# Kernel tuning notes

Hardware: AMD Instinct MI355X
Metric: run time of the kernel (lower is better)

The kernel has to match this reference:

```python
import jax, jax.numpy as jnp
import numpy as np

D_MODEL = 1024
NUM_HEADS = 16
THETA = 10000.0
NEG = -1000000.0  # masked_fill value used by the torch code


def _rope(x, token_positions, theta):
    # x: [B, H, S, d_head]; token_positions: [S] int
    d_k = x.shape[-1]
    half = d_k // 2
    j = jnp.arange(half, dtype=jnp.float32)
    inv_freq = theta ** (-(2.0 * j) / d_k)                      # [half]
    ang = token_positions.astype(jnp.float32)[:, None] * inv_freq  # [S, half]
    cos = jnp.cos(ang)
    sin = jnp.sin(ang)
    xp = x.reshape(x.shape[:-1] + (half, 2))  # adjacent pairs (pc, 2)
    x0, x1 = xp[..., 0], xp[..., 1]
    o0 = x0 * cos - x1 * sin
    o1 = x0 * sin + x1 * cos
    out = jnp.stack([o0, o1], axis=-1)
    return out.reshape(x.shape)


def setup_inputs() -> dict:
    key = jax.random.key(0)
    k0, k1, k2 = jax.random.split(key, 3)
    B, S, D = 2, 2048, D_MODEL
    std = (2.0 / (D + D)) ** 0.5
    X = jax.random.normal(k0, (B, S, D), dtype=jnp.float32)
    QKV_weights = jax.random.normal(k1, (3 * D, D), dtype=jnp.float32) * std
    O_weights = jax.random.normal(k2, (D, D), dtype=jnp.float32) * std
    token_positions = jnp.arange(S, dtype=jnp.int32)
    return {"X": X, "token_positions": token_positions,
            "QKV_weights": QKV_weights, "O_weights": O_weights}


def reference(X, token_positions, QKV_weights, O_weights):
    B, S, D = X.shape
    H = NUM_HEADS
    dh = D // H
    qkv = jnp.einsum('od,bsd->bso', QKV_weights, X)  # [B, S, 3D]
    Q, K, V = jnp.split(qkv, 3, axis=-1)

    def split_heads(t):
        return t.reshape(B, S, H, dh).transpose(0, 2, 1, 3)  # [B,H,S,dh]

    Q, K, V = split_heads(Q), split_heads(K), split_heads(V)
    Q = _rope(Q, token_positions, THETA)
    K = _rope(K, token_positions, THETA)

    scores = (jnp.einsum('bhqd,bhkd->bhqk', Q, K) / jnp.sqrt(jnp.float32(dh))).astype(jnp.float32)
    causal = jnp.tril(jnp.ones((S, S), dtype=bool))
    scores = jnp.where(causal, scores, NEG)
    probs = jax.nn.softmax(scores, axis=-1)
    attn = jnp.einsum('bhqk,bhkd->bhqd', probs, V.astype(jnp.float32)).astype(Q.dtype)
    attn = attn.transpose(0, 2, 1, 3).reshape(B, S, D)
    return jnp.einsum('od,bsd->bso', O_weights, attn)
```

## Files before the change

kernel.cpp:

```cpp
#include <hip/hip_runtime.h>
#include <math.h>

#define S_LEN 2048

using bf16x8  = __attribute__((ext_vector_type(8))) short;
using shortx4 = __attribute__((ext_vector_type(4))) short;
using f32x4   = __attribute__((ext_vector_type(4))) float;
using uintx4  = __attribute__((ext_vector_type(4))) unsigned;
using uintx2  = __attribute__((ext_vector_type(2))) unsigned;

static __device__ __forceinline__ short f2bf(float f) {
  unsigned u = __float_as_uint(f);
  u += 0x7fffu + ((u >> 16) & 1u);
  return (short)(u >> 16);
}

#if __has_builtin(__builtin_amdgcn_cvt_pk_bf16_f32)
using bf16x2_t = __attribute__((ext_vector_type(2))) __bf16;
static __device__ __forceinline__ unsigned pkbf(float a, float b) {
  bf16x2_t v = __builtin_amdgcn_cvt_pk_bf16_f32(a, b);
  return __builtin_bit_cast(unsigned, v);
}
#else
static __device__ __forceinline__ unsigned pkbf(float a, float b) {
  return (unsigned)(unsigned short)f2bf(a) | ((unsigned)(unsigned short)f2bf(b) << 16);
}
#endif

#define GLD_LDS16(gptr, lptr)                                                  \
  __builtin_amdgcn_global_load_lds(                                            \
      (__attribute__((address_space(1))) void*)(gptr),                         \
      (__attribute__((address_space(3))) void*)(lptr), 16, 0, 0)

#define EXP2_SHIFT 20.0f

static __device__ __forceinline__ f32x4 exp2s4(f32x4 a) {
  return (f32x4){__builtin_amdgcn_exp2f(a[0] - EXP2_SHIFT),
                 __builtin_amdgcn_exp2f(a[1] - EXP2_SHIFT),
                 __builtin_amdgcn_exp2f(a[2] - EXP2_SHIFT),
                 __builtin_amdgcn_exp2f(a[3] - EXP2_SHIFT)};
}

static __device__ __forceinline__ int sigma64(int k) {
  return (k & 0x20) | ((k & 0x0C) << 1) | ((k & 0x10) >> 2) | (k & 3);
}

__global__ __launch_bounds__(256) void init_kernel(const float* __restrict__ X,
                                                   const float* __restrict__ W1,
                                                   const float* __restrict__ W2,
                                                   const int* __restrict__ tok,
                                                   short* __restrict__ Xb,
                                                   short* __restrict__ W1b,
                                                   short* __restrict__ W2b,
                                                   float2* __restrict__ table) {
  if (blockIdx.x < 4096) {
    size_t idx = (size_t)(blockIdx.x * 256 + threadIdx.x) * 8;
    const float* src;
    short* dst;
    size_t off;
    if (idx < 4194304) { src = X; dst = Xb; off = idx; }
    else if (idx < 4194304 + 3145728) { src = W1; dst = W1b; off = idx - 4194304; }
    else { src = W2; dst = W2b; off = idx - (4194304 + 3145728); }
    float4 a = *(const float4*)(src + off);
    float4 b = *(const float4*)(src + off + 4);
    bf16x8 o = {f2bf(a.x), f2bf(a.y), f2bf(a.z), f2bf(a.w),
                f2bf(b.x), f2bf(b.y), f2bf(b.z), f2bf(b.w)};
    *(bf16x8*)(dst + off) = o;
  } else {
    int i = (blockIdx.x - 4096) * 256 + threadIdx.x;
    int s = i >> 5, j = i & 31;
    double pos = (double)tok[s];
    double ang = pos * pow(10000.0, -(double)j / 32.0);
    table[i] = make_float2((float)cos(ang), (float)sin(ang));
  }
}

template <int BM, typename OutT, int EPI>
__global__ __launch_bounds__(256) void gemm_ll(const short* __restrict__ A,
                                               const short* __restrict__ B,
                                               OutT* __restrict__ C,
                                               const float2* __restrict__ tab,
                                               short* __restrict__ Qb,
                                               short* __restrict__ Kb,
                                               short* __restrict__ Vb,
                                               int M, int N, int K) {
  constexpr int MI = BM / 32;
  constexpr int AI = BM / 64;
  __shared__ short As[BM * 32];
  __shared__ short Bs[128 * 32];
  const int tid  = threadIdx.x;
  const int lane = tid & 63;
  const int wv   = tid >> 6;
  const int wm   = (wv >> 1) * (BM / 2);
  const int wn   = (wv & 1) * 64;
  const int m16  = lane & 15;
  const int q4   = lane >> 4;
  const int rowBase = blockIdx.y * BM;
  const int colBase = blockIdx.x * 128;
  const int lrow = lane >> 2;
  const int lchk = (lane & 3) ^ ((lane >> 3) & 3);
  const int fsw  = (q4 ^ ((m16 >> 1) & 3)) * 8;

  f32x4 acc[MI][4];
#pragma unroll
  for (int i = 0; i < MI; ++i)
#pragma unroll
    for (int j = 0; j < 4; ++j) acc[i][j] = (f32x4){0.f, 0.f, 0.f, 0.f};

  const short* Agl = A + (size_t)rowBase * K;
  const short* Bgl = B + (size_t)colBase * K;

  for (int kk = 0; kk < K; kk += 32) {
#pragma unroll
    for (int i = 0; i < AI; ++i) {
      const int r0 = (wv * AI + i) * 16;
      GLD_LDS16(Agl + (size_t)(r0 + lrow) * K + kk + lchk * 8, &As[r0 * 32]);
    }
#pragma unroll
    for (int i = 0; i < 2; ++i) {
      const int r0 = (wv * 2 + i) * 16;
      GLD_LDS16(Bgl + (size_t)(r0 + lrow) * K + kk + lchk * 8, &Bs[r0 * 32]);
    }
    __syncthreads();

    bf16x8 af[MI], bfv[4];
#pragma unroll
    for (int mi = 0; mi < MI; ++mi)
      af[mi] = *(const bf16x8*)&As[(wm + mi * 16 + m16) * 32 + fsw];
#pragma unroll
    for (int ni = 0; ni < 4; ++ni)
      bfv[ni] = *(const bf16x8*)&Bs[(wn + ni * 16 + m16) * 32 + fsw];
#pragma unroll
    for (int mi = 0; mi < MI; ++mi)
#pragma unroll
      for (int ni = 0; ni < 4; ++ni)
        acc[mi][ni] = __builtin_amdgcn_mfma_f32_16x16x32_bf16(af[mi], bfv[ni], acc[mi][ni], 0, 0, 0);
    __syncthreads();
  }

  if constexpr (EPI == 0) {
#pragma unroll
    for (int mi = 0; mi < MI; ++mi)
#pragma unroll
      for (int ni = 0; ni < 4; ++ni) {
        const int rbase = rowBase + wm + mi * 16 + q4 * 4;
        const int cidx  = colBase + wn + ni * 16 + m16;
#pragma unroll
        for (int r = 0; r < 4; ++r) {
          float v = acc[mi][ni][r];
          if constexpr (sizeof(OutT) == 2)
            C[(size_t)(rbase + r) * N + cidx] = (OutT)f2bf(v);
          else
            C[(size_t)(rbase + r) * N + cidx] = (OutT)v;
        }
      }
  } else {
    const int sect = colBase >> 10;
#pragma unroll
    for (int mi = 0; mi < MI; ++mi)
#pragma unroll
      for (int ni = 0; ni < 4; ++ni) {
        const int col = colBase + wn + ni * 16 + m16;
        const int rb  = rowBase + wm + mi * 16 + q4 * 4;
        if (sect == 2) {
          const int hd = col - 2048;
#pragma unroll
          for (int r = 0; r < 4; ++r)
            Vb[(size_t)(rb + r) * 1024 + hd] = f2bf(acc[mi][ni][r]);
        } else {
          const int cc = col & 1023;
          const int h = cc >> 6, d = cc & 63, j = d >> 1;
          const float sgn = (m16 & 1) ? 1.f : -1.f;
          short* dstp = (sect == 0) ? Qb : Kb;
          const float scl = (sect == 0) ? (0.125f * 1.44269504f) : 1.f;
#pragma unroll
          for (int r = 0; r < 4; ++r) {
            const int row = rb + r;
            const int s = row & (S_LEN - 1), bidx = row >> 11;
            float2 cs = tab[s * 32 + j];
            float self = acc[mi][ni][r];
            float part = __shfl_xor(self, 1);
            float o = (self * cs.x + sgn * part * cs.y) * scl;
            dstp[((size_t)((bidx * 16 + h) * S_LEN + s)) * 64 + d] = f2bf(o);
          }
        }
      }
  }
}

__global__ __launch_bounds__(256) void prep_v(const short* __restrict__ Vb,
                                              short* __restrict__ VT) {
  __shared__ __align__(16) short VtL[64 * 72];
  const int tid = threadIdx.x;
  const int st  = blockIdx.x, bh = blockIdx.y;
  const int b   = bh >> 4, h = bh & 15;
  const int r   = tid >> 2, seg = tid & 3;
  const int s   = st * 64 + r;
  const int pr  = sigma64(r);
  {
    const short* vsrc = Vb + (size_t)(b * S_LEN + s) * 1024 + h * 64 + seg * 16;
    short in[16];
    *(bf16x8*)&in[0] = ((const bf16x8*)vsrc)[0];
    *(bf16x8*)&in[8] = ((const bf16x8*)vsrc)[1];
#pragma unroll
    for (int d = 0; d < 16; ++d)
      VtL[(seg * 16 + d) * 72 + pr] = in[d];
  }
  __syncthreads();
  short* vdst = VT + ((size_t)bh * 64 + r) * S_LEN + st * 64 + seg * 16;
  ((bf16x8*)vdst)[0] = *(bf16x8*)&VtL[r * 72 + seg * 16];
  ((bf16x8*)vdst)[1] = *(bf16x8*)&VtL[r * 72 + seg * 16 + 8];
}

__global__ __launch_bounds__(256, 2) void attn_mfma(const short* __restrict__ Qb,
                                                    const short* __restrict__ Kb,
                                                    const short* __restrict__ VT,
                                                    short* __restrict__ attnb) {
  __shared__ __align__(16) short Smem[9216];
  short* Ks = Smem;
  short* Vs = Smem + 64 * 72;
  const int tid  = threadIdx.x;
  const int lane = tid & 63;
  const int w    = tid >> 6;
  const int m16  = lane & 15;
  const int q4   = lane >> 4;
  const int bh   = blockIdx.x;
  const int jtx  = blockIdx.y;
  const int jt   = (jtx < 8) ? (15 - jtx) : (jtx - 8);
  const int b    = bh >> 4, h = bh & 15;
  const short* Qh = Qb + (size_t)bh * S_LEN * 64;
  const short* Kh = Kb + (size_t)bh * S_LEN * 64;
  const short* Vh = VT + (size_t)bh * 64 * S_LEN;

  const int srow = tid >> 3;
  const int seg  = tid & 7;

  const bf16x8 ones = {16256, 16256, 16256, 16256, 16256, 16256, 16256, 16256};

  const int q0 = jt * 128;
  const int ktiles = 2 * jt + 2;

  bf16x8 qf[2][2];
#pragma unroll
  for (int n = 0; n < 2; ++n)
#pragma unroll
    for (int ks = 0; ks < 2; ++ks)
      qf[n][ks] = *(const bf16x8*)(Qh + (size_t)(q0 + w * 32 + n * 16 + m16) * 64 + ks * 32 + q4 * 8);

  f32x4 O[2][4], Lacc[2];
#pragma unroll
  for (int n = 0; n < 2; ++n) {
    Lacc[n] = (f32x4){0.f, 0.f, 0.f, 0.f};
#pragma unroll
    for (int c = 0; c < 4; ++c) O[n][c] = (f32x4){0.f, 0.f, 0.f, 0.f};
  }

  bf16x8 kst[2], vst[2];
#pragma unroll
  for (int i = 0; i < 2; ++i) {
    kst[i] = *(const bf16x8*)(Kh + (size_t)(i * 32 + srow) * 64 + seg * 8);
    vst[i] = *(const bf16x8*)(Vh + (size_t)(i * 32 + srow) * S_LEN + seg * 8);
  }

  for (int t = 0; t < ktiles; ++t) {
#pragma unroll
    for (int i = 0; i < 2; ++i) {
      *(bf16x8*)&Ks[(i * 32 + srow) * 72 + seg * 8] = kst[i];
      *(bf16x8*)&Vs[(i * 32 + srow) * 72 + seg * 8] = vst[i];
    }
    __syncthreads();

    if (t + 1 < ktiles) {
#pragma unroll
      for (int i = 0; i < 2; ++i) {
        kst[i] = *(const bf16x8*)(Kh + (size_t)((t + 1) * 64 + i * 32 + srow) * 64 + seg * 8);
        vst[i] = *(const bf16x8*)(Vh + (size_t)(i * 32 + srow) * S_LEN + (t + 1) * 64 + seg * 8);
      }
    }

    f32x4 sc[2][4];
#pragma unroll
    for (int n = 0; n < 2; ++n)
#pragma unroll
      for (int c = 0; c < 4; ++c) sc[n][c] = (f32x4){0.f, 0.f, 0.f, 0.f};
#pragma unroll
    for (int ks = 0; ks < 2; ++ks) {
#pragma unroll
      for (int c = 0; c < 4; ++c) {
        bf16x8 kf = *(const bf16x8*)&Ks[(c * 16 + m16) * 72 + ks * 32 + q4 * 8];
#pragma unroll
        for (int n = 0; n < 2; ++n)
          sc[n][c] = __builtin_amdgcn_mfma_f32_16x16x32_bf16(kf, qf[n][ks], sc[n][c], 0, 0, 0);
      }
    }

    if (t >= ktiles - 2) {
#pragma unroll
      for (int n = 0; n < 2; ++n)
#pragma unroll
        for (int c = 0; c < 4; ++c) {
          const int qg = q0 + w * 32 + n * 16 + m16;
#pragma unroll
          for (int rr = 0; rr < 4; ++rr) {
            const int kg = t * 64 + c * 16 + q4 * 4 + rr;
            if (kg > qg) sc[n][c][rr] = -1e30f;
          }
        }
    }

    bf16x8 pb[2][2];
#pragma unroll
    for (int n = 0; n < 2; ++n) {
#pragma unroll
      for (int c = 0; c < 4; ++c) sc[n][c] = exp2s4(sc[n][c]);
      uintx4 u0 = {pkbf(sc[n][0][0], sc[n][0][1]), pkbf(sc[n][0][2], sc[n][0][3]),
                   pkbf(sc[n][1][0], sc[n][1][1]), pkbf(sc[n][1][2], sc[n][1][3])};
      uintx4 u1 = {pkbf(sc[n][2][0], sc[n][2][1]), pkbf(sc[n][2][2], sc[n][2][3]),
                   pkbf(sc[n][3][0], sc[n][3][1]), pkbf(sc[n][3][2], sc[n][3][3])};
      pb[n][0] = __builtin_bit_cast(bf16x8, u0);
      pb[n][1] = __builtin_bit_cast(bf16x8, u1);
    }

#pragma unroll
    for (int ch = 0; ch < 2; ++ch) {
#pragma unroll
      for (int c2 = 0; c2 < 4; ++c2) {
        bf16x8 va = *(const bf16x8*)&Vs[(c2 * 16 + m16) * 72 + ch * 32 + q4 * 8];
#pragma unroll
        for (int n = 0; n < 2; ++n)
          O[n][c2] = __builtin_amdgcn_mfma_f32_16x16x32_bf16(va, pb[n][ch], O[n][c2], 0, 0, 0);
      }
#pragma unroll
      for (int n = 0; n < 2; ++n)
        Lacc[n] = __builtin_amdgcn_mfma_f32_16x16x32_bf16(ones, pb[n][ch], Lacc[n], 0, 0, 0);
    }
    __syncthreads();
  }

#pragma unroll
  for (int n = 0; n < 2; ++n) {
    const float inv = __frcp_rn(Lacc[n][0]);
#pragma unroll
    for (int c2 = 0; c2 < 4; ++c2) {
      uintx2 uo = {pkbf(O[n][c2][0] * inv, O[n][c2][1] * inv),
                   pkbf(O[n][c2][2] * inv, O[n][c2][3] * inv)};
      *(shortx4*)&Smem[(w * 32 + n * 16 + m16) * 72 + c2 * 16 + q4 * 4] =
          __builtin_bit_cast(shortx4, uo);
    }
  }
  __syncthreads();
  {
    const int row = tid >> 1, hf = tid & 1;
    const short* src = &Smem[row * 72 + hf * 32];
    short* dst = attnb + (size_t)(b * S_LEN + q0 + row) * 1024 + h * 64 + hf * 32;
    ((bf16x8*)dst)[0] = ((const bf16x8*)src)[0];
    ((bf16x8*)dst)[1] = ((const bf16x8*)src)[1];
    ((bf16x8*)dst)[2] = ((const bf16x8*)src)[2];
    ((bf16x8*)dst)[3] = ((const bf16x8*)src)[3];
  }
}

extern "C" void kernel_launch(void* const* d_in, const int* in_sizes, int n_in,
                              void* d_out, int out_size, void* d_ws, size_t ws_size,
                              hipStream_t stream) {
  const float* X    = (const float*)d_in[0];
  const int*   tok  = (const int*)d_in[1];
  const float* Wqkv = (const float*)d_in[2];
  const float* Wo   = (const float*)d_in[3];
  float* out = (float*)d_out;

  char* w = (char*)d_ws;
  float2* table = (float2*)w;
  short*  Qb    = (short*)(w + 524288);
  short*  Kb    = Qb + 4194304;
  short*  VTt   = Kb + 4194304;
  short*  Vb    = VTt + 4194304;
  short*  Xb    = Vb + 4194304;
  short*  Wqkvb = Xb + 4194304;
  short*  Wob   = Wqkvb + 3145728;
  short*  attnb = Wob + 1048576;

  hipLaunchKernelGGL(init_kernel, dim3(4352), dim3(256), 0, stream,
                     X, Wqkv, Wo, tok, Xb, Wqkvb, Wob, table);
  hipLaunchKernelGGL((gemm_ll<128, short, 1>), dim3(24, 32), dim3(256), 0, stream,
                     Xb, Wqkvb, (short*)nullptr, table, Qb, Kb, Vb, 4096, 3072, 1024);
  hipLaunchKernelGGL(prep_v, dim3(32, 32), dim3(256), 0, stream, Vb, VTt);
  hipLaunchKernelGGL(attn_mfma, dim3(32, 16), dim3(256), 0, stream,
                     Qb, Kb, VTt, attnb);
  hipLaunchKernelGGL((gemm_ll<64, float, 0>), dim3(8, 64), dim3(256), 0, stream,
                     attnb, Wob, out, (const float2*)nullptr,
                     (short*)nullptr, (short*)nullptr, (short*)nullptr,
                     4096, 1024, 1024);
}
```

Measured before the change: 184.8 us.

## Replace QKV projection GEMM with 256x256-tile, 4-stage pipelined 512-thread kernel

Adds a dedicated QKV projection kernel that computes 256x256 output tiles with 8 waves. It uses a 4-deep LDS ring filled by direct global-to-LDS loads, XOR-swizzled fragment reads, and interleaved MFMA phases with priority hints and explicit waitcnt. Workgroup indices are remapped so neighbouring blocks share tiles. The goal is more data reuse per tile and hiding global-load latency behind MFMA work. The trade-offs are 128KB of LDS per block and only 192 blocks, which may leave some CUs idle. The RoPE and scaling epilogue is kept but writes single shorts with scattered stores.

```diff
diff --git a/kernel.cpp b/kernel.cpp
--- a/kernel.cpp
+++ b/kernel.cpp
@@ -75,6 +75,148 @@
   }
 }
 
+__global__ __launch_bounds__(512, 2) void gemm256_qkv(const short* __restrict__ A,
+                                                      const short* __restrict__ B,
+                                                      const float2* __restrict__ tab,
+                                                      short* __restrict__ Qb,
+                                                      short* __restrict__ Kb,
+                                                      short* __restrict__ Vb) {
+  constexpr int K = 1024;
+  constexpr int NT = K / 32;
+  __shared__ short smem[65536];
+
+  const int tid  = threadIdx.x;
+  const int lane = tid & 63;
+  const int wv   = tid >> 6;
+  const int m16  = lane & 15;
+  const int q4   = lane >> 4;
+
+  const int wg  = blockIdx.x;
+  const int wgs = (wg & 7) * 24 + (wg >> 3);
+  const int cx  = wgs % 12, cy = wgs / 12;
+  const int rowBase = cy * 256;
+  const int colBase = cx * 256;
+
+  const int wmr = (wv >> 2) * 128;
+  const int wnr = (wv & 3) * 64;
+
+  const int lrow = lane >> 2;
+  const int lchk = (lane & 3) ^ ((lane >> 3) & 3);
+  const int fsw  = (q4 ^ ((m16 >> 1) & 3)) * 8;
+
+  const short* Agl = A + (size_t)rowBase * K;
+  const short* Bgl = B + (size_t)colBase * K;
+
+  const short* Ath0 = Agl + (size_t)((wv * 2 + 0) * 16 + lrow) * K + lchk * 8;
+  const short* Ath1 = Agl + (size_t)((wv * 2 + 1) * 16 + lrow) * K + lchk * 8;
+  const short* Bth0 = Bgl + (size_t)((wv * 2 + 0) * 16 + lrow) * K + lchk * 8;
+  const short* Bth1 = Bgl + (size_t)((wv * 2 + 1) * 16 + lrow) * K + lchk * 8;
+  const int lA0 = wv * 1024;
+  const int lA1 = wv * 1024 + 512;
+
+#define STAGE_A(s)                                                             \
+  do {                                                                         \
+    const int _sl = ((s) & 3) * 8192;                                          \
+    GLD_LDS16(Ath0 + (size_t)(s) * 32, &smem[_sl + lA0]);                      \
+    GLD_LDS16(Ath1 + (size_t)(s) * 32, &smem[_sl + lA1]);                      \
+  } while (0)
+#define STAGE_B(s)                                                             \
+  do {                                                                         \
+    const int _sl = 32768 + ((s) & 3) * 8192;                                  \
+    GLD_LDS16(Bth0 + (size_t)(s) * 32, &smem[_sl + lA0]);                      \
+    GLD_LDS16(Bth1 + (size_t)(s) * 32, &smem[_sl + lA1]);                      \
+  } while (0)
+
+  f32x4 acc[8][4];
+#pragma unroll
+  for (int i = 0; i < 8; ++i)
+#pragma unroll
+    for (int j = 0; j < 4; ++j) acc[i][j] = (f32x4){0.f, 0.f, 0.f, 0.f};
+
+  STAGE_A(0); STAGE_B(0);
+  STAGE_A(1); STAGE_B(1);
+  STAGE_A(2); STAGE_B(2);
+  asm volatile("s_waitcnt vmcnt(8)" ::: "memory");
+  __builtin_amdgcn_s_barrier();
+  __builtin_amdgcn_sched_barrier(0);
+
+  for (int t = 0; t < NT; ++t) {
+    const short* As = &smem[(t & 3) * 8192];
+    const short* Bs = &smem[32768 + (t & 3) * 8192];
+
+    bf16x8 bF[4], aF0[4], aF1[4];
+#pragma unroll
+    for (int ni = 0; ni < 4; ++ni)
+      bF[ni] = *(const bf16x8*)&Bs[(wnr + ni * 16 + m16) * 32 + fsw];
+#pragma unroll
+    for (int mi = 0; mi < 4; ++mi)
+      aF0[mi] = *(const bf16x8*)&As[(wmr + mi * 16 + m16) * 32 + fsw];
+    if (t + 3 < NT) STAGE_A(t + 3);
+    __builtin_amdgcn_s_barrier();
+    __builtin_amdgcn_s_setprio(1);
+#pragma unroll
+    for (int mi = 0; mi < 4; ++mi)
+#pragma unroll
+      for (int ni = 0; ni < 4; ++ni)
+        acc[mi][ni] = __builtin_amdgcn_mfma_f32_16x16x32_bf16(aF0[mi], bF[ni], acc[mi][ni], 0, 0, 0);
+    __builtin_amdgcn_s_setprio(0);
+    __builtin_amdgcn_s_barrier();
+
+#pragma unroll
+    for (int mi = 0; mi < 4; ++mi)
+      aF1[mi] = *(const bf16x8*)&As[(wmr + (mi + 4) * 16 + m16) * 32 + fsw];
+    if (t + 3 < NT) STAGE_B(t + 3);
+    __builtin_amdgcn_s_barrier();
+    __builtin_amdgcn_s_setprio(1);
+#pragma unroll
+    for (int mi = 0; mi < 4; ++mi)
+#pragma unroll
+      for (int ni = 0; ni < 4; ++ni)
+        acc[mi + 4][ni] = __builtin_amdgcn_mfma_f32_16x16x32_bf16(aF1[mi], bF[ni], acc[mi + 4][ni], 0, 0, 0);
+    __builtin_amdgcn_s_setprio(0);
+
+    const int rem = NT - 1 - t;
+    if (rem >= 3)      asm volatile("s_waitcnt vmcnt(8)" ::: "memory");
+    else if (rem == 2) asm volatile("s_waitcnt vmcnt(4)" ::: "memory");
+    else if (rem == 1) asm volatile("s_waitcnt vmcnt(0)" ::: "memory");
+    __builtin_amdgcn_s_barrier();
+    __builtin_amdgcn_sched_barrier(0);
+  }
+#undef STAGE_A
+#undef STAGE_B
+
+  const int sect = colBase >> 10;
+#pragma unroll
+  for (int mi = 0; mi < 8; ++mi)
+#pragma unroll
+    for (int ni = 0; ni < 4; ++ni) {
+      const int col = colBase + wnr + ni * 16 + m16;
+      const int rb  = rowBase + wmr + mi * 16 + q4 * 4;
+      if (sect == 2) {
+        const int hd = col - 2048;
+#pragma unroll
+        for (int r = 0; r < 4; ++r)
+          Vb[(size_t)(rb + r) * 1024 + hd] = f2bf(acc[mi][ni][r]);
+      } else {
+        const int cc = col & 1023;
+        const int h = cc >> 6, d = cc & 63, j = d >> 1;
+        const float sgn = (m16 & 1) ? 1.f : -1.f;
+        short* dstp = (sect == 0) ? Qb : Kb;
+        const float scl = (sect == 0) ? (0.125f * 1.44269504f) : 1.f;
+#pragma unroll
+        for (int r = 0; r < 4; ++r) {
+          const int row = rb + r;
+          const int s = row & (S_LEN - 1), bidx = row >> 11;
+          float2 cs = tab[s * 32 + j];
+          float self = acc[mi][ni][r];
+          float part = __shfl_xor(self, 1);
+          float o = (self * cs.x + sgn * part * cs.y) * scl;
+          dstp[((size_t)((bidx * 16 + h) * S_LEN + s)) * 64 + d] = f2bf(o);
+        }
+      }
+    }
+}
+
 template <int BM, typename OutT, int EPI>
 __global__ __launch_bounds__(256) void gemm_ll(const short* __restrict__ A,
                                                const short* __restrict__ B,
@@ -382,8 +524,8 @@
 
   hipLaunchKernelGGL(init_kernel, dim3(4352), dim3(256), 0, stream,
                      X, Wqkv, Wo, tok, Xb, Wqkvb, Wob, table);
-  hipLaunchKernelGGL((gemm_ll<128, short, 1>), dim3(24, 32), dim3(256), 0, stream,
-                     Xb, Wqkvb, (short*)nullptr, table, Qb, Kb, Vb, 4096, 3072, 1024);
+  hipLaunchKernelGGL(gemm256_qkv, dim3(192), dim3(512), 0, stream,
+                     Xb, Wqkvb, table, Qb, Kb, Vb);
   hipLaunchKernelGGL(prep_v, dim3(32, 32), dim3(256), 0, stream, Vb, VTt);
   hipLaunchKernelGGL(attn_mfma, dim3(32, 16), dim3(256), 0, stream,
                      Qb, Kb, VTt, attnb);
```

Result: no change. 187.3 us (+1.4%).

## Fuse V transpose into QKV GEMM epilogue, remap blocks, enlarge output GEMM tile

Applied to the files above, without the earlier changes.

The QKV GEMM epilogue now writes V straight into the transposed, sigma-permuted layout that attention reads, so the separate prep_v kernel and its intermediate V buffer go away. Workgroup IDs are remapped across groups of 8, presumably to spread tiles across XCDs or improve cache locality. The output projection switches from a 64-row tile to a 128-row tile, halving its grid. The transposed V stores are scattered 4-element writes with stride S_LEN, which may coalesce worse than the old row-wise stores.

```diff
diff --git a/kernel.cpp b/kernel.cpp
--- a/kernel.cpp
+++ b/kernel.cpp
@@ -82,7 +82,7 @@
                                                const float2* __restrict__ tab,
                                                short* __restrict__ Qb,
                                                short* __restrict__ Kb,
-                                               short* __restrict__ Vb,
+                                               short* __restrict__ VT,
                                                int M, int N, int K) {
   constexpr int MI = BM / 32;
   constexpr int AI = BM / 64;
@@ -95,8 +95,13 @@
   const int wn   = (wv & 1) * 64;
   const int m16  = lane & 15;
   const int q4   = lane >> 4;
-  const int rowBase = blockIdx.y * BM;
-  const int colBase = blockIdx.x * 128;
+
+  const int nwg = gridDim.x * gridDim.y;
+  int bid = blockIdx.y * gridDim.x + blockIdx.x;
+  bid = (bid & 7) * (nwg >> 3) + (bid >> 3);
+  const int rowBase = (bid / gridDim.x) * BM;
+  const int colBase = (bid % gridDim.x) * 128;
+
   const int lrow = lane >> 2;
   const int lchk = (lane & 3) ^ ((lane >> 3) & 3);
   const int fsw  = (q4 ^ ((m16 >> 1) & 3)) * 8;
@@ -164,9 +169,12 @@
         const int rb  = rowBase + wm + mi * 16 + q4 * 4;
         if (sect == 2) {
           const int hd = col - 2048;
-#pragma unroll
-          for (int r = 0; r < 4; ++r)
-            Vb[(size_t)(rb + r) * 1024 + hd] = f2bf(acc[mi][ni][r]);
+          const int h = hd >> 6, d = hd & 63;
+          const int b = rb >> 11, s0 = rb & (S_LEN - 1);
+          shortx4 pk4 = {f2bf(acc[mi][ni][0]), f2bf(acc[mi][ni][1]),
+                         f2bf(acc[mi][ni][2]), f2bf(acc[mi][ni][3])};
+          *(shortx4*)(VT + ((size_t)((b * 16 + h) * 64 + d)) * S_LEN +
+                      (s0 & ~63) + sigma64(s0 & 63)) = pk4;
         } else {
           const int cc = col & 1023;
           const int h = cc >> 6, d = cc & 63, j = d >> 1;
@@ -186,30 +194,6 @@
         }
       }
   }
-}
-
-__global__ __launch_bounds__(256) void prep_v(const short* __restrict__ Vb,
-                                              short* __restrict__ VT) {
-  __shared__ __align__(16) short VtL[64 * 72];
-  const int tid = threadIdx.x;
-  const int st  = blockIdx.x, bh = blockIdx.y;
-  const int b   = bh >> 4, h = bh & 15;
-  const int r   = tid >> 2, seg = tid & 3;
-  const int s   = st * 64 + r;
-  const int pr  = sigma64(r);
-  {
-    const short* vsrc = Vb + (size_t)(b * S_LEN + s) * 1024 + h * 64 + seg * 16;
-    short in[16];
-    *(bf16x8*)&in[0] = ((const bf16x8*)vsrc)[0];
-    *(bf16x8*)&in[8] = ((const bf16x8*)vsrc)[1];
-#pragma unroll
-    for (int d = 0; d < 16; ++d)
-      VtL[(seg * 16 + d) * 72 + pr] = in[d];
-  }
-  __syncthreads();
-  short* vdst = VT + ((size_t)bh * 64 + r) * S_LEN + st * 64 + seg * 16;
-  ((bf16x8*)vdst)[0] = *(bf16x8*)&VtL[r * 72 + seg * 16];
-  ((bf16x8*)vdst)[1] = *(bf16x8*)&VtL[r * 72 + seg * 16 + 8];
 }
 
 __global__ __launch_bounds__(256, 2) void attn_mfma(const short* __restrict__ Qb,
@@ -374,8 +358,7 @@
   short*  Qb    = (short*)(w + 524288);
   short*  Kb    = Qb + 4194304;
   short*  VTt   = Kb + 4194304;
-  short*  Vb    = VTt + 4194304;
-  short*  Xb    = Vb + 4194304;
+  short*  Xb    = VTt + 2 * 4194304;
   short*  Wqkvb = Xb + 4194304;
   short*  Wob   = Wqkvb + 3145728;
   short*  attnb = Wob + 1048576;
@@ -383,11 +366,10 @@
   hipLaunchKernelGGL(init_kernel, dim3(4352), dim3(256), 0, stream,
                      X, Wqkv, Wo, tok, Xb, Wqkvb, Wob, table);
   hipLaunchKernelGGL((gemm_ll<128, short, 1>), dim3(24, 32), dim3(256), 0, stream,
-                     Xb, Wqkvb, (short*)nullptr, table, Qb, Kb, Vb, 4096, 3072, 1024);
-  hipLaunchKernelGGL(prep_v, dim3(32, 32), dim3(256), 0, stream, Vb, VTt);
+                     Xb, Wqkvb, (short*)nullptr, table, Qb, Kb, VTt, 4096, 3072, 1024);
   hipLaunchKernelGGL(attn_mfma, dim3(32, 16), dim3(256), 0, stream,
                      Qb, Kb, VTt, attnb);
-  hipLaunchKernelGGL((gemm_ll<64, float, 0>), dim3(8, 64), dim3(256), 0, stream,
+  hipLaunchKernelGGL((gemm_ll<128, float, 0>), dim3(8, 32), dim3(256), 0, stream,
                      attnb, Wob, out, (const float2*)nullptr,
                      (short*)nullptr, (short*)nullptr, (short*)nullptr,
                      4096, 1024, 1024);
```

Result: no change. 184.3 us (-0.3%).
